# Performance work log

Hardware: AMD Instinct MI355X
Metric: run time of the kernel (lower is better)

The kernel has to match this reference:

```python
import jax, jax.numpy as jnp
import numpy as np

NEG_SLOPE = 0.2


def _gat_conv(x, src, dst, W, a_src, a_dst, b, n_nodes):
    # Single-head PyG GATConv (normalize arg in source is ignored by GATConv).
    h = x @ W                                   # [N, C_out]
    e_src = h @ a_src                           # [N] alpha_src contribution
    e_dst = h @ a_dst                           # [N] alpha_dst contribution
    logits = jax.nn.leaky_relu(e_src[src] + e_dst[dst], NEG_SLOPE)  # [E]
    m = jax.ops.segment_max(logits, dst, num_segments=n_nodes)      # per-dst max
    e = jnp.exp(logits - m[dst])
    denom = jax.ops.segment_sum(e, dst, num_segments=n_nodes)
    alpha = e / denom[dst]                      # edge softmax over in-neighbors
    out = jax.ops.segment_sum(h[src] * alpha[:, None], dst, num_segments=n_nodes)
    return out + b


def _add_self_loops(edge_index, n_nodes):
    loop = jnp.arange(n_nodes, dtype=edge_index.dtype)
    src = jnp.concatenate([edge_index[0], loop])
    dst = jnp.concatenate([edge_index[1], loop])
    return src, dst


def setup_inputs() -> dict:
    key = jax.random.key(0)
    ks = jax.random.split(key, 16)
    N, E, C_IN, C_HID, C_OUT = 50000, 1600000, 128, 128, 64
    x = jax.random.normal(ks[0], (N, C_IN), dtype=jnp.float32)
    edge_index = jax.random.randint(ks[1], (2, E), 0, N, dtype=jnp.int32)
    glorot = lambda k, shape: jax.random.normal(k, shape, jnp.float32) * np.sqrt(2.0 / sum(shape))
    return {
        "x": x,
        "edge_index": edge_index,
        "W0": glorot(ks[2], (C_IN, C_HID)),
        "as0": glorot(ks[3], (C_HID,)) * 0.1,
        "ad0": glorot(ks[4], (C_HID,)) * 0.1,
        "b0": jnp.zeros((C_HID,), jnp.float32),
        "W1": glorot(ks[5], (C_HID, C_HID)),
        "as1": glorot(ks[6], (C_HID,)) * 0.1,
        "ad1": glorot(ks[7], (C_HID,)) * 0.1,
        "b1": jnp.zeros((C_HID,), jnp.float32),
        "W2": glorot(ks[8], (C_HID, C_OUT)),
        "as2": glorot(ks[9], (C_OUT,)) * 0.1,
        "ad2": glorot(ks[10], (C_OUT,)) * 0.1,
        "b2": jnp.zeros((C_OUT,), jnp.float32),
    }


def reference(x, edge_index, W0, as0, ad0, b0, W1, as1, ad1, b1, W2, as2, ad2, b2):
    n_nodes = x.shape[0]
    src, dst = _add_self_loops(edge_index, n_nodes)
    # eval mode: F.dropout with training=False is identity
    h = jax.nn.relu(_gat_conv(x, src, dst, W0, as0, ad0, b0, n_nodes))
    h = jax.nn.relu(_gat_conv(h, src, dst, W1, as1, ad1, b1, n_nodes))
    out = _gat_conv(h, src, dst, W2, as2, ad2, b2, n_nodes)
    return out
```

## Files before the change

### kernel.cpp

```cpp
#include <hip/hip_runtime.h>
#include <hip/hip_bf16.h>
#include <type_traits>

#define DEVFN __device__ __forceinline__

typedef __attribute__((ext_vector_type(8))) short bfrag;
typedef __attribute__((ext_vector_type(4))) float facc4;

DEVFN float lrelu(float v) { return (v >= 0.f) ? v : 0.2f * v; }

DEVFN float2 bf2x2(unsigned u) {
  return make_float2(__uint_as_float(u << 16), __uint_as_float(u & 0xFFFF0000u));
}
DEVFN float bf_lo(unsigned u) { return __uint_as_float(u << 16); }
DEVFN float bf_hi(unsigned u) { return __uint_as_float(u & 0xFFFF0000u); }
DEVFN unsigned short f2bf(float f) {
  __hip_bfloat16 h = __float2bfloat16(f);
  return *reinterpret_cast<unsigned short*>(&h);
}
DEVFN unsigned packbf2(float x, float y) {
  return (unsigned)f2bf(x) | ((unsigned)f2bf(y) << 16);
}

DEVFN float wave_sum(float v) {
#pragma unroll
  for (int o = 1; o < 64; o <<= 1) v += __shfl_xor(v, o, 64);
  return v;
}
DEVFN float wave_max(float v) {
#pragma unroll
  for (int o = 1; o < 64; o <<= 1) v = fmaxf(v, __shfl_xor(v, o, 64));
  return v;
}

template<int C, bool A_FP32>
__global__ __launch_bounds__(256) void gemm_mfma(const void* __restrict__ Xin,
                                                 const float* __restrict__ W,
                                                 const float* __restrict__ a_src,
                                                 const float* __restrict__ a_dst,
                                                 unsigned short* __restrict__ H,
                                                 float* __restrict__ es,
                                                 float* __restrict__ ed,
                                                 int N) {
  constexpr int K = 128;
  constexpr int LSTR = K + 8;
  constexpr int NT = C / 16;
  __shared__ unsigned short WsT[C * LSTR];

  const int t = threadIdx.x;
  for (int i = t; i < K * C; i += 256) {
    int k = i / C;
    int c = i - k * C;
    WsT[c * LSTR + k] = f2bf(W[i]);
  }
  __syncthreads();

  const int wave = t >> 6;
  const int lane = t & 63;
  const int l15 = lane & 15;
  const int quad = lane >> 4;
  const int arow = blockIdx.x * 64 + wave * 16 + l15;
  const bool avalid = arow < N;

  facc4 acc[NT];
#pragma unroll
  for (int i = 0; i < NT; ++i) acc[i] = (facc4){0.f, 0.f, 0.f, 0.f};

#pragma unroll
  for (int ks = 0; ks < 4; ++ks) {
    bfrag a;
    if (A_FP32) {
      if (avalid) {
        const float* xp = (const float*)Xin + (size_t)arow * K + quad * 8 + ks * 32;
        float4 u = *(const float4*)xp;
        float4 v = *(const float4*)(xp + 4);
        a[0] = (short)f2bf(u.x); a[1] = (short)f2bf(u.y);
        a[2] = (short)f2bf(u.z); a[3] = (short)f2bf(u.w);
        a[4] = (short)f2bf(v.x); a[5] = (short)f2bf(v.y);
        a[6] = (short)f2bf(v.z); a[7] = (short)f2bf(v.w);
      } else {
        a = (bfrag){0, 0, 0, 0, 0, 0, 0, 0};
      }
    } else {
      const unsigned short* xp =
          (const unsigned short*)Xin + (size_t)arow * K + quad * 8 + ks * 32;
      a = *(const bfrag*)xp;
    }
#pragma unroll
    for (int ct = 0; ct < NT; ++ct) {
      bfrag b = *(const bfrag*)(&WsT[(ct * 16 + l15) * LSTR + ks * 32 + quad * 8]);
      acc[ct] = __builtin_amdgcn_mfma_f32_16x16x32_bf16(a, b, acc[ct], 0, 0, 0);
    }
  }

  float asv[NT], adv[NT];
#pragma unroll
  for (int ct = 0; ct < NT; ++ct) {
    asv[ct] = a_src[ct * 16 + l15];
    adv[ct] = a_dst[ct * 16 + l15];
  }

  const int orow0 = blockIdx.x * 64 + wave * 16 + quad * 4;
#pragma unroll
  for (int r = 0; r < 4; ++r) {
    const int orow = orow0 + r;
    float ps = 0.f, pd = 0.f;
#pragma unroll
    for (int ct = 0; ct < NT; ++ct) {
      if (orow < N) H[(size_t)orow * C + ct * 16 + l15] = f2bf(acc[ct][r]);
      ps += acc[ct][r] * asv[ct];
      pd += acc[ct][r] * adv[ct];
    }
#pragma unroll
    for (int msk = 1; msk < 16; msk <<= 1) {
      ps += __shfl_xor(ps, msk, 64);
      pd += __shfl_xor(pd, msk, 64);
    }
    if (l15 == 0 && orow < N) { es[orow] = ps; ed[orow] = pd; }
  }
}

__global__ void hist_only(const int* __restrict__ dst, int* __restrict__ hmat,
                          int E, int nbk, int chunk) {
  __shared__ int hist[4 * 128];
  const int t = threadIdx.x;
  for (int i = t; i < 4 * 128; i += 256) hist[i] = 0;
  __syncthreads();
  int* h = &hist[(t >> 6) << 7];
  const int e0 = blockIdx.x * chunk;
  const int e1 = min(E, e0 + chunk);
  for (int e = e0 + t; e < e1; e += 256) {
    atomicAdd(&h[dst[e] >> 9], 1);
  }
  __syncthreads();
  if (t < nbk)
    hmat[t * gridDim.x + blockIdx.x] =
        hist[t] + hist[t + 128] + hist[t + 256] + hist[t + 384];
}

__global__ void scan_partial(const int* __restrict__ in, int* __restrict__ csum, int n) {
  __shared__ int sh[256];
  int i = blockIdx.x * 256 + threadIdx.x;
  sh[threadIdx.x] = (i < n) ? in[i] : 0;
  __syncthreads();
  for (int o = 128; o > 0; o >>= 1) {
    if (threadIdx.x < o) sh[threadIdx.x] += sh[threadIdx.x + o];
    __syncthreads();
  }
  if (threadIdx.x == 0) csum[blockIdx.x] = sh[0];
}

__global__ void scan_chunks(int* __restrict__ csum, int nch) {
  __shared__ int sh[256];
  __shared__ int carry;
  if (threadIdx.x == 0) carry = 0;
  __syncthreads();
  for (int base = 0; base < nch; base += 256) {
    int i = base + threadIdx.x;
    int v = (i < nch) ? csum[i] : 0;
    sh[threadIdx.x] = v;
    __syncthreads();
    for (int o = 1; o < 256; o <<= 1) {
      int t = (threadIdx.x >= o) ? sh[threadIdx.x - o] : 0;
      __syncthreads();
      sh[threadIdx.x] += t;
      __syncthreads();
    }
    if (i < nch) csum[i] = carry + sh[threadIdx.x] - v;
    __syncthreads();
    if (threadIdx.x == 255) carry += sh[255];
    __syncthreads();
  }
}

__global__ void scan_final(const int* __restrict__ deg, const int* __restrict__ csum,
                           int* __restrict__ rp, int* __restrict__ wp, int N, int E) {
  __shared__ int sh[256];
  int i = blockIdx.x * 256 + threadIdx.x;
  int v = (i < N) ? deg[i] : 0;
  sh[threadIdx.x] = v;
  __syncthreads();
  for (int o = 1; o < 256; o <<= 1) {
    int t = (threadIdx.x >= o) ? sh[threadIdx.x - o] : 0;
    __syncthreads();
    sh[threadIdx.x] += t;
    __syncthreads();
  }
  if (i < N) {
    int r = csum[blockIdx.x] + sh[threadIdx.x] - v;
    rp[i] = r;
    wp[i] = r;
  }
  if (blockIdx.x == 0 && threadIdx.x == 0) rp[N] = E;
}

__global__ void scan_final_excl(const int* __restrict__ in, const int* __restrict__ csum,
                                int* __restrict__ out, int n) {
  __shared__ int sh[256];
  int i = blockIdx.x * 256 + threadIdx.x;
  int v = (i < n) ? in[i] : 0;
  sh[threadIdx.x] = v;
  __syncthreads();
  for (int o = 1; o < 256; o <<= 1) {
    int t = (threadIdx.x >= o) ? sh[threadIdx.x - o] : 0;
    __syncthreads();
    sh[threadIdx.x] += t;
    __syncthreads();
  }
  if (i < n) out[i] = csum[blockIdx.x] + sh[threadIdx.x] - v;
}

__global__ void place_pass(const int* __restrict__ src, const int* __restrict__ dst,
                           const int* __restrict__ off, int2* __restrict__ be,
                           int E, int nbk, int chunk) {
  __shared__ int cur[128];
  const int t = threadIdx.x;
  if (t < nbk) cur[t] = off[t * gridDim.x + blockIdx.x];
  __syncthreads();
  const int e0 = blockIdx.x * chunk;
  const int e1 = min(E, e0 + chunk);
  for (int e = e0 + t; e < e1; e += 256) {
    int d = dst[e];
    int s = src[e];
    int p = atomicAdd(&cur[d >> 9], 1);
    be[p] = make_int2(s, d);
  }
}

__global__ void bucket_final(const int2* __restrict__ be, const int* __restrict__ off,
                             int* __restrict__ rp, unsigned short* __restrict__ col,
                             int E, int N, int nbk, int pblk) {
  __shared__ int cur[512];
  __shared__ int ps[256];
  const int b = blockIdx.x;
  const int n0 = b << 9;
  const int cnt = min(512, N - n0);
  const int t = threadIdx.x;
  for (int i = t; i < cnt; i += 256) cur[i] = 0;
  __syncthreads();
  const int e0 = off[b * pblk];
  const int e1 = (b + 1 < nbk) ? off[(b + 1) * pblk] : E;
  for (int e = e0 + t; e < e1; e += 256) {
    int2 sd = be[e];
    atomicAdd(&cur[sd.y - n0], 1);
  }
  __syncthreads();
  const int i0 = 2 * t, i1 = 2 * t + 1;
  const int v0 = (i0 < cnt) ? cur[i0] : 0;
  const int v1 = (i1 < cnt) ? cur[i1] : 0;
  ps[t] = v0 + v1;
  __syncthreads();
  for (int o = 1; o < 256; o <<= 1) {
    int u = (t >= o) ? ps[t - o] : 0;
    __syncthreads();
    ps[t] += u;
    __syncthreads();
  }
  const int base = e0 + ps[t] - (v0 + v1);
  if (i0 < cnt) { rp[n0 + i0] = base;      cur[i0] = base; }
  if (i1 < cnt) { rp[n0 + i1] = base + v0; cur[i1] = base + v0; }
  if (b == nbk - 1 && t == 0) rp[N] = E;
  __syncthreads();
  for (int e = e0 + t; e < e1; e += 256) {
    int2 sd = be[e];
    int p = atomicAdd(&cur[sd.y - n0], 1);
    col[p] = (unsigned short)sd.x;
  }
}

__global__ void csr_scatter_ranged(const int* __restrict__ src,
                                   const int* __restrict__ dst,
                                   int* __restrict__ wp, int* __restrict__ col,
                                   int E, int range, int npass) {
  const int stride = gridDim.x * blockDim.x;
  const int gid = blockIdx.x * blockDim.x + threadIdx.x;
  for (int pass = 0; pass < npass; ++pass) {
    const int lo = pass * range;
    const int hi = lo + range;
    for (int e = gid; e < E; e += stride) {
      int d = dst[e];
      if (d >= lo && d < hi) {
        int p = atomicAdd(wp + d, 1);
        col[p] = src[e];
      }
    }
  }
}

__global__ void csr_count(const int* __restrict__ dst, int* __restrict__ deg, int E) {
  int e = blockIdx.x * blockDim.x + threadIdx.x;
  if (e < E) atomicAdd(deg + dst[e], 1);
}

template<bool RELU, typename IT>
__global__ void gat_fused128(const int* __restrict__ row_ptr,
                             const IT* __restrict__ col,
                             const float* __restrict__ es,
                             const float* __restrict__ ed,
                             const unsigned short* __restrict__ H,
                             const float* __restrict__ bias,
                             void* __restrict__ outX, int N) {
  const int lane = threadIdx.x & 63;
  const int n = blockIdx.x * (blockDim.x >> 6) + (threadIdx.x >> 6);
  if (n >= N) return;

  const int g4 = lane >> 4;
  const int l15 = lane & 15;

  const int k0 = row_ptr[n];
  const int k1 = row_ptr[n + 1];
  const int deg = k1 - k0;
  const float edd = ed[n];
  const float self_lg = lrelu(es[n] + edd);

  const char* Hb = (const char*)H;
  float acc[8];
#pragma unroll
  for (int i = 0; i < 8; ++i) acc[i] = 0.f;
  float den, sp;

  if (deg <= 64) {
    int k = k0 + lane;
    bool act = (k < k1);
    int c = act ? (int)col[k] : 0;
    float lg = act ? lrelu(es[c] + edd) : -3.0e38f;
    float m = fmaxf(wave_max(lg), self_lg);
    float p = act ? __expf(lg - m) : 0.f;
    sp = __expf(self_lg - m);
    den = wave_sum(p) + sp;
    for (int j = 0; j < deg; j += 8) {
      int i0 = min(j + g4, 63);
      int i1 = min(j + 4 + g4, 63);
      int c0 = __shfl(c, i0);
      int c1 = __shfl(c, i1);
      float p0 = __shfl(p, i0);
      float p1 = __shfl(p, i1);
      uint4 v0 = *(const uint4*)(Hb + (((size_t)c0 << 8) + l15 * 16));
      uint4 v1 = *(const uint4*)(Hb + (((size_t)c1 << 8) + l15 * 16));
      acc[0] += p0 * bf_lo(v0.x); acc[1] += p0 * bf_hi(v0.x);
      acc[2] += p0 * bf_lo(v0.y); acc[3] += p0 * bf_hi(v0.y);
      acc[4] += p0 * bf_lo(v0.z); acc[5] += p0 * bf_hi(v0.z);
      acc[6] += p0 * bf_lo(v0.w); acc[7] += p0 * bf_hi(v0.w);
      acc[0] += p1 * bf_lo(v1.x); acc[1] += p1 * bf_hi(v1.x);
      acc[2] += p1 * bf_lo(v1.y); acc[3] += p1 * bf_hi(v1.y);
      acc[4] += p1 * bf_lo(v1.z); acc[5] += p1 * bf_hi(v1.z);
      acc[6] += p1 * bf_lo(v1.w); acc[7] += p1 * bf_hi(v1.w);
    }
  } else {
    float mloc = self_lg;
    for (int base = k0; base < k1; base += 64) {
      int k = base + lane;
      if (k < k1) mloc = fmaxf(mloc, lrelu(es[(int)col[k]] + edd));
    }
    float m = wave_max(mloc);
    sp = __expf(self_lg - m);
    den = sp;
    for (int base = k0; base < k1; base += 64) {
      int k = base + lane;
      bool act = (k < k1);
      int c = act ? (int)col[k] : 0;
      float p = act ? __expf(lrelu(es[c] + edd) - m) : 0.f;
      den += wave_sum(p);
      int len = min(64, k1 - base);
      for (int j = 0; j < len; j += 8) {
        int i0 = min(j + g4, 63);
        int i1 = min(j + 4 + g4, 63);
        int c0 = __shfl(c, i0);
        int c1 = __shfl(c, i1);
        float p0 = __shfl(p, i0);
        float p1 = __shfl(p, i1);
        uint4 v0 = *(const uint4*)(Hb + (((size_t)c0 << 8) + l15 * 16));
        uint4 v1 = *(const uint4*)(Hb + (((size_t)c1 << 8) + l15 * 16));
        acc[0] += p0 * bf_lo(v0.x); acc[1] += p0 * bf_hi(v0.x);
        acc[2] += p0 * bf_lo(v0.y); acc[3] += p0 * bf_hi(v0.y);
        acc[4] += p0 * bf_lo(v0.z); acc[5] += p0 * bf_hi(v0.z);
        acc[6] += p0 * bf_lo(v0.w); acc[7] += p0 * bf_hi(v0.w);
        acc[0] += p1 * bf_lo(v1.x); acc[1] += p1 * bf_hi(v1.x);
        acc[2] += p1 * bf_lo(v1.y); acc[3] += p1 * bf_hi(v1.y);
        acc[4] += p1 * bf_lo(v1.z); acc[5] += p1 * bf_hi(v1.z);
        acc[6] += p1 * bf_lo(v1.w); acc[7] += p1 * bf_hi(v1.w);
      }
    }
  }

#pragma unroll
  for (int i = 0; i < 8; ++i) {
    acc[i] += __shfl_xor(acc[i], 16, 64);
    acc[i] += __shfl_xor(acc[i], 32, 64);
  }

  uint4 hv = *(const uint4*)(Hb + (((size_t)n << 8) + l15 * 16));
  acc[0] += sp * bf_lo(hv.x); acc[1] += sp * bf_hi(hv.x);
  acc[2] += sp * bf_lo(hv.y); acc[3] += sp * bf_hi(hv.y);
  acc[4] += sp * bf_lo(hv.z); acc[5] += sp * bf_hi(hv.z);
  acc[6] += sp * bf_lo(hv.w); acc[7] += sp * bf_hi(hv.w);

  float inv = 1.f / den;
  float4 bv0 = *(const float4*)(bias + l15 * 8);
  float4 bv1 = *(const float4*)(bias + l15 * 8 + 4);
  float o0 = acc[0] * inv + bv0.x, o1 = acc[1] * inv + bv0.y;
  float o2 = acc[2] * inv + bv0.z, o3 = acc[3] * inv + bv0.w;
  float o4 = acc[4] * inv + bv1.x, o5 = acc[5] * inv + bv1.y;
  float o6 = acc[6] * inv + bv1.z, o7 = acc[7] * inv + bv1.w;
  if (RELU) {
    o0 = fmaxf(o0, 0.f); o1 = fmaxf(o1, 0.f); o2 = fmaxf(o2, 0.f);
    o3 = fmaxf(o3, 0.f); o4 = fmaxf(o4, 0.f); o5 = fmaxf(o5, 0.f);
    o6 = fmaxf(o6, 0.f); o7 = fmaxf(o7, 0.f);
  }
  if (g4 == 0) {
    uint4 w;
    w.x = packbf2(o0, o1); w.y = packbf2(o2, o3);
    w.z = packbf2(o4, o5); w.w = packbf2(o6, o7);
    *(uint4*)((char*)outX + (((size_t)n << 8) + l15 * 16)) = w;
  }
}

template<bool RELU, typename IT>
__global__ void gat_fused64(const int* __restrict__ row_ptr,
                            const IT* __restrict__ col,
                            const float* __restrict__ es,
                            const float* __restrict__ ed,
                            const unsigned short* __restrict__ H,
                            const float* __restrict__ bias,
                            float* __restrict__ outX, int N) {
  const int lane = threadIdx.x & 63;
  const int n = blockIdx.x * (blockDim.x >> 6) + (threadIdx.x >> 6);
  if (n >= N) return;

  const int g8 = lane >> 3;
  const int l8 = lane & 7;

  const int k0 = row_ptr[n];
  const int k1 = row_ptr[n + 1];
  const int deg = k1 - k0;
  const float edd = ed[n];
  const float self_lg = lrelu(es[n] + edd);

  const char* Hb = (const char*)H;
  float acc[8];
#pragma unroll
  for (int i = 0; i < 8; ++i) acc[i] = 0.f;
  float den, sp;

  if (deg <= 64) {
    int k = k0 + lane;
    bool act = (k < k1);
    int c = act ? (int)col[k] : 0;
    float lg = act ? lrelu(es[c] + edd) : -3.0e38f;
    float m = fmaxf(wave_max(lg), self_lg);
    float p = act ? __expf(lg - m) : 0.f;
    sp = __expf(self_lg - m);
    den = wave_sum(p) + sp;
    for (int j = 0; j < deg; j += 8) {
      int i0 = min(j + g8, 63);
      int c0 = __shfl(c, i0);
      float p0 = __shfl(p, i0);
      uint4 v0 = *(const uint4*)(Hb + (((size_t)c0 << 7) + l8 * 16));
      acc[0] += p0 * bf_lo(v0.x); acc[1] += p0 * bf_hi(v0.x);
      acc[2] += p0 * bf_lo(v0.y); acc[3] += p0 * bf_hi(v0.y);
      acc[4] += p0 * bf_lo(v0.z); acc[5] += p0 * bf_hi(v0.z);
      acc[6] += p0 * bf_lo(v0.w); acc[7] += p0 * bf_hi(v0.w);
    }
  } else {
    float mloc = self_lg;
    for (int base = k0; base < k1; base += 64) {
      int k = base + lane;
      if (k < k1) mloc = fmaxf(mloc, lrelu(es[(int)col[k]] + edd));
    }
    float m = wave_max(mloc);
    sp = __expf(self_lg - m);
    den = sp;
    for (int base = k0; base < k1; base += 64) {
      int k = base + lane;
      bool act = (k < k1);
      int c = act ? (int)col[k] : 0;
      float p = act ? __expf(lrelu(es[c] + edd) - m) : 0.f;
      den += wave_sum(p);
      int len = min(64, k1 - base);
      for (int j = 0; j < len; j += 8) {
        int i0 = min(j + g8, 63);
        int c0 = __shfl(c, i0);
        float p0 = __shfl(p, i0);
        uint4 v0 = *(const uint4*)(Hb + (((size_t)c0 << 7) + l8 * 16));
        acc[0] += p0 * bf_lo(v0.x); acc[1] += p0 * bf_hi(v0.x);
        acc[2] += p0 * bf_lo(v0.y); acc[3] += p0 * bf_hi(v0.y);
        acc[4] += p0 * bf_lo(v0.z); acc[5] += p0 * bf_hi(v0.z);
        acc[6] += p0 * bf_lo(v0.w); acc[7] += p0 * bf_hi(v0.w);
      }
    }
  }

#pragma unroll
  for (int i = 0; i < 8; ++i) {
    acc[i] += __shfl_xor(acc[i], 8, 64);
    acc[i] += __shfl_xor(acc[i], 16, 64);
    acc[i] += __shfl_xor(acc[i], 32, 64);
  }

  uint4 hv = *(const uint4*)(Hb + (((size_t)n << 7) + l8 * 16));
  acc[0] += sp * bf_lo(hv.x); acc[1] += sp * bf_hi(hv.x);
  acc[2] += sp * bf_lo(hv.y); acc[3] += sp * bf_hi(hv.y);
  acc[4] += sp * bf_lo(hv.z); acc[5] += sp * bf_hi(hv.z);
  acc[6] += sp * bf_lo(hv.w); acc[7] += sp * bf_hi(hv.w);

  float inv = 1.f / den;
  float4 bv0 = *(const float4*)(bias + l8 * 8);
  float4 bv1 = *(const float4*)(bias + l8 * 8 + 4);
  float4 w0, w1;
  w0.x = acc[0] * inv + bv0.x; w0.y = acc[1] * inv + bv0.y;
  w0.z = acc[2] * inv + bv0.z; w0.w = acc[3] * inv + bv0.w;
  w1.x = acc[4] * inv + bv1.x; w1.y = acc[5] * inv + bv1.y;
  w1.z = acc[6] * inv + bv1.z; w1.w = acc[7] * inv + bv1.w;
  if (RELU) {
    w0.x = fmaxf(w0.x, 0.f); w0.y = fmaxf(w0.y, 0.f);
    w0.z = fmaxf(w0.z, 0.f); w0.w = fmaxf(w0.w, 0.f);
    w1.x = fmaxf(w1.x, 0.f); w1.y = fmaxf(w1.y, 0.f);
    w1.z = fmaxf(w1.z, 0.f); w1.w = fmaxf(w1.w, 0.f);
  }
  if (g8 == 0) {
    char* op = (char*)outX + (((size_t)n << 8) + l8 * 32);
    *(float4*)op = w0;
    *(float4*)(op + 16) = w1;
  }
}


extern "C" void kernel_launch(void* const* d_in, const int* in_sizes, int n_in,
                              void* d_out, int out_size, void* d_ws, size_t ws_size,
                              hipStream_t stream) {
  const int C_HID = in_sizes[3];
  const int C_FIN = in_sizes[11];
  const int C_IN  = in_sizes[2] / C_HID;
  const int N     = in_sizes[0] / C_IN;
  const int E     = in_sizes[1] / 2;
  const int NPAD  = ((N + 63) / 64) * 64;

  const float* x = (const float*)d_in[0];
  const int* ei  = (const int*)d_in[1];
  const int* src = ei;
  const int* dst = ei + E;

  const float* W0  = (const float*)d_in[2];
  const float* as0 = (const float*)d_in[3];
  const float* ad0 = (const float*)d_in[4];
  const float* b0  = (const float*)d_in[5];
  const float* W1  = (const float*)d_in[6];
  const float* as1 = (const float*)d_in[7];
  const float* ad1 = (const float*)d_in[8];
  const float* b1  = (const float*)d_in[9];
  const float* W2  = (const float*)d_in[10];
  const float* as2 = (const float*)d_in[11];
  const float* ad2 = (const float*)d_in[12];
  const float* b2  = (const float*)d_in[13];

  char* base = (char*)d_ws;
  size_t off = 0;
  auto alloc = [&](size_t bytes) -> char* {
    char* p = base + off;
    off = (off + bytes + 255) & ~((size_t)255);
    return p;
  };
  const int PBLK = 512;
  const int NBK  = (N + 511) >> 9;
  const int M    = NBK * PBLK;
  const int NCH  = (N + 255) / 256;
  const int MCH  = (M + 255) / 256;
  const int SCH  = (NCH > MCH ? NCH : MCH);

  unsigned short* XB  = (unsigned short*)alloc((size_t)NPAD * C_HID * 2);
  unsigned short* H   = (unsigned short*)alloc((size_t)N * C_HID * 2);
  float* ES    = (float*)alloc((size_t)N * sizeof(float));
  float* ED    = (float*)alloc((size_t)N * sizeof(float));
  int*   RP    = (int*)alloc((size_t)(N + 1) * sizeof(int));
  int*   WP    = (int*)alloc((size_t)N * sizeof(int));
  void*  COL   = (void*)alloc((size_t)E * sizeof(int));
  int*   DEG   = (int*)alloc((size_t)N * sizeof(int));
  int*   CSUM  = (int*)alloc((size_t)SCH * sizeof(int));
  int*   HMAT  = (int*)alloc((size_t)M * sizeof(int));
  int*   OFF   = (int*)alloc((size_t)M * sizeof(int));
  int2*  BE    = (int2*)alloc((size_t)E * sizeof(int2));
  (void)ws_size;

  const int wgrid = (N + 3) / 4;
  const int mgrid = NPAD / 64;
  const bool u16 = (N <= 65535);

  if (u16) {
    const int CHUNK = (E + PBLK - 1) / PBLK;
    hist_only<<<PBLK, 256, 0, stream>>>(dst, HMAT, E, NBK, CHUNK);
    scan_partial<<<MCH, 256, 0, stream>>>(HMAT, CSUM, M);
    scan_chunks<<<1, 256, 0, stream>>>(CSUM, MCH);
    scan_final_excl<<<MCH, 256, 0, stream>>>(HMAT, CSUM, OFF, M);
    place_pass<<<PBLK, 256, 0, stream>>>(src, dst, OFF, BE, E, NBK, CHUNK);
    bucket_final<<<NBK, 256, 0, stream>>>(BE, OFF, RP, (unsigned short*)COL,
                                          E, N, NBK, PBLK);
  } else {
    hipMemsetAsync(DEG, 0, (size_t)N * sizeof(int), stream);
    const int ET256 = (E + 255) / 256;
    csr_count<<<ET256, 256, 0, stream>>>(dst, DEG, E);
    scan_partial<<<NCH, 256, 0, stream>>>(DEG, CSUM, N);
    scan_chunks<<<1, 256, 0, stream>>>(CSUM, NCH);
    scan_final<<<NCH, 256, 0, stream>>>(DEG, CSUM, RP, WP, N, E);
    const int NPASS = 8;
    const int range = (N + NPASS - 1) / NPASS;
    csr_scatter_ranged<<<2048, 256, 0, stream>>>(src, dst, WP, (int*)COL, E,
                                                 range, NPASS);
  }

  auto run_layers = [&](auto* col) {
    using IT = typename std::remove_pointer<decltype(col)>::type;
    gemm_mfma<128, true><<<mgrid, 256, 0, stream>>>(x, W0, as0, ad0, H, ES, ED, N);
    gat_fused128<true, IT><<<wgrid, 256, 0, stream>>>(RP, col, ES, ED, H, b0, XB, N);
    gemm_mfma<128, false><<<mgrid, 256, 0, stream>>>(XB, W1, as1, ad1, H, ES, ED, N);
    gat_fused128<true, IT><<<wgrid, 256, 0, stream>>>(RP, col, ES, ED, H, b1, XB, N);
    gemm_mfma<64, false><<<mgrid, 256, 0, stream>>>(XB, W2, as2, ad2, H, ES, ED, N);
    gat_fused64<false, IT><<<wgrid, 256, 0, stream>>>(RP, col, ES, ED, H, b2,
                                                      (float*)d_out, N);
  };

  if (u16) run_layers((unsigned short*)COL);
  else     run_layers((int*)COL);
  (void)out_size; (void)n_in;
}
```

Baseline: 332.2 us.

## Split GAT aggregation into separate edge-softmax and packed-FMA gather kernels

Each fused GAT aggregation kernel becomes two kernels per layer. The first computes per-edge softmax numerators into a new E-sized buffer, plus the inverse denominator and self-loop weight per node. The second gathers H rows weighted by these precomputed values, using 2-wide float vector FMAs and a partial unroll. This is meant to take exp/max work and es gathers off the latency-bound gather loop, but it adds extra launches and an extra write and read of the P array per layer.

After: 369.5 us. 11.2% more time.

```diff
diff --git a/kernel.cpp b/kernel.cpp
--- a/kernel.cpp
+++ b/kernel.cpp
@@ -6,14 +6,15 @@
 
 typedef __attribute__((ext_vector_type(8))) short bfrag;
 typedef __attribute__((ext_vector_type(4))) float facc4;
+typedef __attribute__((ext_vector_type(2))) float f32x2;
 
 DEVFN float lrelu(float v) { return (v >= 0.f) ? v : 0.2f * v; }
 
-DEVFN float2 bf2x2(unsigned u) {
-  return make_float2(__uint_as_float(u << 16), __uint_as_float(u & 0xFFFF0000u));
-}
 DEVFN float bf_lo(unsigned u) { return __uint_as_float(u << 16); }
 DEVFN float bf_hi(unsigned u) { return __uint_as_float(u & 0xFFFF0000u); }
+DEVFN f32x2 upk2(unsigned u) {
+  f32x2 r; r.x = bf_lo(u); r.y = bf_hi(u); return r;
+}
 DEVFN unsigned short f2bf(float f) {
   __hip_bfloat16 h = __float2bfloat16(f);
   return *reinterpret_cast<unsigned short*>(&h);
@@ -32,6 +33,15 @@
   for (int o = 1; o < 64; o <<= 1) v = fmaxf(v, __shfl_xor(v, o, 64));
   return v;
 }
+
+#define FMA_ROW(p_, v_)                                                  \
+  {                                                                      \
+    f32x2 pv; pv.x = (p_); pv.y = (p_);                                  \
+    acc2[0] += pv * upk2((v_).x);                                        \
+    acc2[1] += pv * upk2((v_).y);                                        \
+    acc2[2] += pv * upk2((v_).z);                                        \
+    acc2[3] += pv * upk2((v_).w);                                        \
+  }
 
 template<int C, bool A_FP32>
 __global__ __launch_bounds__(256) void gemm_mfma(const void* __restrict__ Xin,
@@ -292,32 +302,23 @@
   if (e < E) atomicAdd(deg + dst[e], 1);
 }
 
-template<bool RELU, typename IT>
-__global__ void gat_fused128(const int* __restrict__ row_ptr,
-                             const IT* __restrict__ col,
-                             const float* __restrict__ es,
-                             const float* __restrict__ ed,
-                             const unsigned short* __restrict__ H,
-                             const float* __restrict__ bias,
-                             void* __restrict__ outX, int N) {
+template<typename IT>
+__global__ void gat_alpha(const int* __restrict__ row_ptr,
+                          const IT* __restrict__ col,
+                          const float* __restrict__ es,
+                          const float* __restrict__ ed,
+                          float* __restrict__ P,
+                          float* __restrict__ DENI,
+                          float* __restrict__ SPV, int N) {
   const int lane = threadIdx.x & 63;
   const int n = blockIdx.x * (blockDim.x >> 6) + (threadIdx.x >> 6);
   if (n >= N) return;
-
-  const int g4 = lane >> 4;
-  const int l15 = lane & 15;
 
   const int k0 = row_ptr[n];
   const int k1 = row_ptr[n + 1];
   const int deg = k1 - k0;
   const float edd = ed[n];
   const float self_lg = lrelu(es[n] + edd);
-
-  const char* Hb = (const char*)H;
-  float acc[8];
-#pragma unroll
-  for (int i = 0; i < 8; ++i) acc[i] = 0.f;
-  float den, sp;
 
   if (deg <= 64) {
     int k = k0 + lane;
@@ -326,8 +327,63 @@
     float lg = act ? lrelu(es[c] + edd) : -3.0e38f;
     float m = fmaxf(wave_max(lg), self_lg);
     float p = act ? __expf(lg - m) : 0.f;
-    sp = __expf(self_lg - m);
-    den = wave_sum(p) + sp;
+    float sp = __expf(self_lg - m);
+    float den = wave_sum(p) + sp;
+    if (act) P[k] = p;
+    if (lane == 0) { DENI[n] = 1.f / den; SPV[n] = sp; }
+  } else {
+    float mloc = self_lg;
+    for (int base = k0; base < k1; base += 64) {
+      int k = base + lane;
+      if (k < k1) mloc = fmaxf(mloc, lrelu(es[(int)col[k]] + edd));
+    }
+    float m = wave_max(mloc);
+    float sp = __expf(self_lg - m);
+    float den = sp;
+    for (int base = k0; base < k1; base += 64) {
+      int k = base + lane;
+      bool act = (k < k1);
+      float p = act ? __expf(lrelu(es[(int)col[k]] + edd) - m) : 0.f;
+      den += wave_sum(p);
+      if (act) P[k] = p;
+    }
+    if (lane == 0) { DENI[n] = 1.f / den; SPV[n] = sp; }
+  }
+}
+
+template<bool RELU, typename IT>
+__global__ void gat_gather128(const int* __restrict__ row_ptr,
+                              const IT* __restrict__ col,
+                              const float* __restrict__ P,
+                              const float* __restrict__ DENI,
+                              const float* __restrict__ SPV,
+                              const unsigned short* __restrict__ H,
+                              const float* __restrict__ bias,
+                              void* __restrict__ outX, int N) {
+  const int lane = threadIdx.x & 63;
+  const int n = blockIdx.x * (blockDim.x >> 6) + (threadIdx.x >> 6);
+  if (n >= N) return;
+
+  const int g4 = lane >> 4;
+  const int l15 = lane & 15;
+
+  const int k0 = row_ptr[n];
+  const int k1 = row_ptr[n + 1];
+  const int deg = k1 - k0;
+  const float sp = SPV[n];
+  const float inv = DENI[n];
+
+  const char* Hb = (const char*)H;
+  f32x2 acc2[4];
+#pragma unroll
+  for (int i = 0; i < 4; ++i) { acc2[i].x = 0.f; acc2[i].y = 0.f; }
+
+  if (deg <= 64) {
+    int k = k0 + lane;
+    bool act = (k < k1);
+    int c = act ? (int)col[k] : 0;
+    float p = act ? P[k] : 0.f;
+#pragma unroll 2
     for (int j = 0; j < deg; j += 8) {
       int i0 = min(j + g4, 63);
       int i1 = min(j + 4 + g4, 63);
@@ -337,31 +393,17 @@
       float p1 = __shfl(p, i1);
       uint4 v0 = *(const uint4*)(Hb + (((size_t)c0 << 8) + l15 * 16));
       uint4 v1 = *(const uint4*)(Hb + (((size_t)c1 << 8) + l15 * 16));
-      acc[0] += p0 * bf_lo(v0.x); acc[1] += p0 * bf_hi(v0.x);
-      acc[2] += p0 * bf_lo(v0.y); acc[3] += p0 * bf_hi(v0.y);
-      acc[4] += p0 * bf_lo(v0.z); acc[5] += p0 * bf_hi(v0.z);
-      acc[6] += p0 * bf_lo(v0.w); acc[7] += p0 * bf_hi(v0.w);
-      acc[0] += p1 * bf_lo(v1.x); acc[1] += p1 * bf_hi(v1.x);
-      acc[2] += p1 * bf_lo(v1.y); acc[3] += p1 * bf_hi(v1.y);
-      acc[4] += p1 * bf_lo(v1.z); acc[5] += p1 * bf_hi(v1.z);
-      acc[6] += p1 * bf_lo(v1.w); acc[7] += p1 * bf_hi(v1.w);
+      FMA_ROW(p0, v0);
+      FMA_ROW(p1, v1);
     }
   } else {
-    float mloc = self_lg;
-    for (int base = k0; base < k1; base += 64) {
-      int k = base + lane;
-      if (k < k1) mloc = fmaxf(mloc, lrelu(es[(int)col[k]] + edd));
-    }
-    float m = wave_max(mloc);
-    sp = __expf(self_lg - m);
-    den = sp;
     for (int base = k0; base < k1; base += 64) {
       int k = base + lane;
       bool act = (k < k1);
       int c = act ? (int)col[k] : 0;
-      float p = act ? __expf(lrelu(es[c] + edd) - m) : 0.f;
-      den += wave_sum(p);
+      float p = act ? P[k] : 0.f;
       int len = min(64, k1 - base);
+#pragma unroll 2
       for (int j = 0; j < len; j += 8) {
         int i0 = min(j + g4, 63);
         int i1 = min(j + 4 + g4, 63);
@@ -371,37 +413,33 @@
         float p1 = __shfl(p, i1);
         uint4 v0 = *(const uint4*)(Hb + (((size_t)c0 << 8) + l15 * 16));
         uint4 v1 = *(const uint4*)(Hb + (((size_t)c1 << 8) + l15 * 16));
-        acc[0] += p0 * bf_lo(v0.x); acc[1] += p0 * bf_hi(v0.x);
-        acc[2] += p0 * bf_lo(v0.y); acc[3] += p0 * bf_hi(v0.y);
-        acc[4] += p0 * bf_lo(v0.z); acc[5] += p0 * bf_hi(v0.z);
-        acc[6] += p0 * bf_lo(v0.w); acc[7] += p0 * bf_hi(v0.w);
-        acc[0] += p1 * bf_lo(v1.x); acc[1] += p1 * bf_hi(v1.x);
-        acc[2] += p1 * bf_lo(v1.y); acc[3] += p1 * bf_hi(v1.y);
-        acc[4] += p1 * bf_lo(v1.z); acc[5] += p1 * bf_hi(v1.z);
-        acc[6] += p1 * bf_lo(v1.w); acc[7] += p1 * bf_hi(v1.w);
+        FMA_ROW(p0, v0);
+        FMA_ROW(p1, v1);
       }
     }
   }
 
+  float a[8];
+#pragma unroll
+  for (int i = 0; i < 4; ++i) { a[2 * i] = acc2[i].x; a[2 * i + 1] = acc2[i].y; }
 #pragma unroll
   for (int i = 0; i < 8; ++i) {
-    acc[i] += __shfl_xor(acc[i], 16, 64);
-    acc[i] += __shfl_xor(acc[i], 32, 64);
+    a[i] += __shfl_xor(a[i], 16, 64);
+    a[i] += __shfl_xor(a[i], 32, 64);
   }
 
   uint4 hv = *(const uint4*)(Hb + (((size_t)n << 8) + l15 * 16));
-  acc[0] += sp * bf_lo(hv.x); acc[1] += sp * bf_hi(hv.x);
-  acc[2] += sp * bf_lo(hv.y); acc[3] += sp * bf_hi(hv.y);
-  acc[4] += sp * bf_lo(hv.z); acc[5] += sp * bf_hi(hv.z);
-  acc[6] += sp * bf_lo(hv.w); acc[7] += sp * bf_hi(hv.w);
-
-  float inv = 1.f / den;
+  a[0] += sp * bf_lo(hv.x); a[1] += sp * bf_hi(hv.x);
+  a[2] += sp * bf_lo(hv.y); a[3] += sp * bf_hi(hv.y);
+  a[4] += sp * bf_lo(hv.z); a[5] += sp * bf_hi(hv.z);
+  a[6] += sp * bf_lo(hv.w); a[7] += sp * bf_hi(hv.w);
+
   float4 bv0 = *(const float4*)(bias + l15 * 8);
   float4 bv1 = *(const float4*)(bias + l15 * 8 + 4);
-  float o0 = acc[0] * inv + bv0.x, o1 = acc[1] * inv + bv0.y;
-  float o2 = acc[2] * inv + bv0.z, o3 = acc[3] * inv + bv0.w;
-  float o4 = acc[4] * inv + bv1.x, o5 = acc[5] * inv + bv1.y;
-  float o6 = acc[6] * inv + bv1.z, o7 = acc[7] * inv + bv1.w;
+  float o0 = a[0] * inv + bv0.x, o1 = a[1] * inv + bv0.y;
+  float o2 = a[2] * inv + bv0.z, o3 = a[3] * inv + bv0.w;
+  float o4 = a[4] * inv + bv1.x, o5 = a[5] * inv + bv1.y;
+  float o6 = a[6] * inv + bv1.z, o7 = a[7] * inv + bv1.w;
   if (RELU) {
     o0 = fmaxf(o0, 0.f); o1 = fmaxf(o1, 0.f); o2 = fmaxf(o2, 0.f);
     o3 = fmaxf(o3, 0.f); o4 = fmaxf(o4, 0.f); o5 = fmaxf(o5, 0.f);
@@ -416,13 +454,14 @@
 }
 
 template<bool RELU, typename IT>
-__global__ void gat_fused64(const int* __restrict__ row_ptr,
-                            const IT* __restrict__ col,
-                            const float* __restrict__ es,
-                            const float* __restrict__ ed,
-                            const unsigned short* __restrict__ H,
-                            const float* __restrict__ bias,
-                            float* __restrict__ outX, int N) {
+__global__ void gat_gather64(const int* __restrict__ row_ptr,
+                             const IT* __restrict__ col,
+                             const float* __restrict__ P,
+                             const float* __restrict__ DENI,
+                             const float* __restrict__ SPV,
+                             const unsigned short* __restrict__ H,
+                             const float* __restrict__ bias,
+                             float* __restrict__ outX, int N) {
   const int lane = threadIdx.x & 63;
   const int n = blockIdx.x * (blockDim.x >> 6) + (threadIdx.x >> 6);
   if (n >= N) return;
@@ -433,84 +472,68 @@
   const int k0 = row_ptr[n];
   const int k1 = row_ptr[n + 1];
   const int deg = k1 - k0;
-  const float edd = ed[n];
-  const float self_lg = lrelu(es[n] + edd);
+  const float sp = SPV[n];
+  const float inv = DENI[n];
 
   const char* Hb = (const char*)H;
-  float acc[8];
-#pragma unroll
-  for (int i = 0; i < 8; ++i) acc[i] = 0.f;
-  float den, sp;
+  f32x2 acc2[4];
+#pragma unroll
+  for (int i = 0; i < 4; ++i) { acc2[i].x = 0.f; acc2[i].y = 0.f; }
 
   if (deg <= 64) {
     int k = k0 + lane;
     bool act = (k < k1);
     int c = act ? (int)col[k] : 0;
-    float lg = act ? lrelu(es[c] + edd) : -3.0e38f;
-    float m = fmaxf(wave_max(lg), self_lg);
-    float p = act ? __expf(lg - m) : 0.f;
-    sp = __expf(self_lg - m);
-    den = wave_sum(p) + sp;
+    float p = act ? P[k] : 0.f;
+#pragma unroll 2
     for (int j = 0; j < deg; j += 8) {
       int i0 = min(j + g8, 63);
       int c0 = __shfl(c, i0);
       float p0 = __shfl(p, i0);
       uint4 v0 = *(const uint4*)(Hb + (((size_t)c0 << 7) + l8 * 16));
-      acc[0] += p0 * bf_lo(v0.x); acc[1] += p0 * bf_hi(v0.x);
-      acc[2] += p0 * bf_lo(v0.y); acc[3] += p0 * bf_hi(v0.y);
-      acc[4] += p0 * bf_lo(v0.z); acc[5] += p0 * bf_hi(v0.z);
-      acc[6] += p0 * bf_lo(v0.w); acc[7] += p0 * bf_hi(v0.w);
+      FMA_ROW(p0, v0);
     }
   } else {
-    float mloc = self_lg;
-    for (int base = k0; base < k1; base += 64) {
-      int k = base + lane;
-      if (k < k1) mloc = fmaxf(mloc, lrelu(es[(int)col[k]] + edd));
-    }
-    float m = wave_max(mloc);
-    sp = __expf(self_lg - m);
-    den = sp;
     for (int base = k0; base < k1; base += 64) {
       int k = base + lane;
       bool act = (k < k1);
       int c = act ? (int)col[k] : 0;
-      float p = act ? __expf(lrelu(es[c] + edd) - m) : 0.f;
-      den += wave_sum(p);
+      float p = act ? P[k] : 0.f;
       int len = min(64, k1 - base);
+#pragma unroll 2
       for (int j = 0; j < len; j += 8) {
         int i0 = min(j + g8, 63);
         int c0 = __shfl(c, i0);
         float p0 = __shfl(p, i0);
         uint4 v0 = *(const uint4*)(Hb + (((size_t)c0 << 7) + l8 * 16));
-        acc[0] += p0 * bf_lo(v0.x); acc[1] += p0 * bf_hi(v0.x);
-        acc[2] += p0 * bf_lo(v0.y); acc[3] += p0 * bf_hi(v0.y);
-        acc[4] += p0 * bf_lo(v0.z); acc[5] += p0 * bf_hi(v0.z);
-        acc[6] += p0 * bf_lo(v0.w); acc[7] += p0 * bf_hi(v0.w);
+        FMA_ROW(p0, v0);
       }
     }
   }
 
+  float a[8];
+#pragma unroll
+  for (int i = 0; i < 4; ++i) { a[2 * i] = acc2[i].x; a[2 * i + 1] = acc2[i].y; }
 #pragma unroll
   for (int i = 0; i < 8; ++i) {
-    acc[i] += __shfl_xor(acc[i], 8, 64);
-    acc[i] += __shfl_xor(acc[i], 16, 64);
-    acc[i] += __shfl_xor(acc[i], 32, 64);
+    a[i] += __shfl_xor(a[i], 8, 64);
+    a[i] += __shfl_xor(a[i], 16, 64);
+    a[i] += __shfl_xor(a[i], 32, 64);
   }
 
   uint4 hv = *(const uint4*)(Hb + (((size_t)n << 7) + l8 * 16));
-  acc[0] += sp * bf_lo(hv.x); acc[1] += sp * bf_hi(hv.x);
-  acc[2] += sp * bf_lo(hv.y); acc[3] += sp * bf_hi(hv.y);
-  acc[4] += sp * bf_lo(hv.z); acc[5] += sp * bf_hi(hv.z);
-  acc[6] += sp * bf_lo(hv.w); acc[7] += sp * bf_hi(hv.w);
-
-  float inv = 1.f / den;
+  a[0] += sp * bf_lo(hv.x); a[1] += sp * bf_hi(hv.x);
+  a[2] += sp * bf_lo(hv.y); a[3] += sp * bf_hi(hv.y);
+  a[4] += sp * bf_lo(hv.z); a[5] += sp * bf_hi(hv.z);
+  a[6] += sp * bf_lo(hv.w); a[7] += sp * bf_hi(hv.w);
+
   float4 bv0 = *(const float4*)(bias + l8 * 8);
   float4 bv1 = *(const float4*)(bias + l8 * 8 + 4);
   float4 w0, w1;
-  w0.x = acc[0] * inv + bv0.x; w0.y = acc[1] * inv + bv0.y;
-  w0.z = acc[2] * inv + bv0.z; w0.w = acc[3] * inv + bv0.w;
-  w1.x = acc[4] * inv + bv1.x; w1.y = acc[5] * inv + bv1.y;
-  w1.z = acc[6] * inv + bv1.z; w1.w = acc[7] * inv + bv1.w;
+  w0.x = a[0] * inv + bv0.x; w0.y = a[1] * inv + bv0.y;
+  w0.z = a[2] * inv + bv0.z; w0.w = a[3] * inv + bv0.w;
+  w1.x = a[4] * inv + bv1.x; w1.y = a[5] * inv + bv1.y;
+  w1.z = a[6] * inv + bv1.z; w1.w = a[7] * inv + bv1.w;
   if (RELU) {
     w0.x = fmaxf(w0.x, 0.f); w0.y = fmaxf(w0.y, 0.f);
     w0.z = fmaxf(w0.z, 0.f); w0.w = fmaxf(w0.w, 0.f);
@@ -571,6 +594,9 @@
   unsigned short* H   = (unsigned short*)alloc((size_t)N * C_HID * 2);
   float* ES    = (float*)alloc((size_t)N * sizeof(float));
   float* ED    = (float*)alloc((size_t)N * sizeof(float));
+  float* P     = (float*)alloc((size_t)E * sizeof(float));
+  float* DENI  = (float*)alloc((size_t)N * sizeof(float));
+  float* SPV   = (float*)alloc((size_t)N * sizeof(float));
   int*   RP    = (int*)alloc((size_t)(N + 1) * sizeof(int));
   int*   WP    = (int*)alloc((size_t)N * sizeof(int));
   void*  COL   = (void*)alloc((size_t)E * sizeof(int));
@@ -610,12 +636,17 @@
   auto run_layers = [&](auto* col) {
     using IT = typename std::remove_pointer<decltype(col)>::type;
     gemm_mfma<128, true><<<mgrid, 256, 0, stream>>>(x, W0, as0, ad0, H, ES, ED, N);
-    gat_fused128<true, IT><<<wgrid, 256, 0, stream>>>(RP, col, ES, ED, H, b0, XB, N);
+    gat_alpha<IT><<<wgrid, 256, 0, stream>>>(RP, col, ES, ED, P, DENI, SPV, N);
+    gat_gather128<true, IT><<<wgrid, 256, 0, stream>>>(RP, col, P, DENI, SPV,
+                                                       H, b0, XB, N);
     gemm_mfma<128, false><<<mgrid, 256, 0, stream>>>(XB, W1, as1, ad1, H, ES, ED, N);
-    gat_fused128<true, IT><<<wgrid, 256, 0, stream>>>(RP, col, ES, ED, H, b1, XB, N);
+    gat_alpha<IT><<<wgrid, 256, 0, stream>>>(RP, col, ES, ED, P, DENI, SPV, N);
+    gat_gather128<true, IT><<<wgrid, 256, 0, stream>>>(RP, col, P, DENI, SPV,
+                                                       H, b1, XB, N);
     gemm_mfma<64, false><<<mgrid, 256, 0, stream>>>(XB, W2, as2, ad2, H, ES, ED, N);
-    gat_fused64<false, IT><<<wgrid, 256, 0, stream>>>(RP, col, ES, ED, H, b2,
-                                                      (float*)d_out, N);
+    gat_alpha<IT><<<wgrid, 256, 0, stream>>>(RP, col, ES, ED, P, DENI, SPV, N);
+    gat_gather64<false, IT><<<wgrid, 256, 0, stream>>>(RP, col, P, DENI, SPV,
+                                                       H, b2, (float*)d_out, N);
   };
 
   if (u16) run_layers((unsigned short*)COL);
```
